# Kernel optimization log

Hardware: AMD Instinct MI355X
Metric: run time of the kernel (lower is better)

The kernel has to match this reference:

```python
import jax, jax.numpy as jnp
import numpy as np

BATCH = 65536
INPUT_DIM = 128
NUM_KNOTS = 10
DEGREE = 3  # n_basis = NUM_KNOTS - DEGREE - 1 = 6


def bspline_basis(x, knots, degree):
    """Cox-de Boor B-spline basis, vectorized over all batch/feature entries.

    x: [B, D] (already clipped into [knots[0], knots[-1]))
    knots: [K] uniform knot vector
    returns: [B, D, K - degree - 1]
    """
    xe = x[..., None]                                            # [B, D, 1]
    # degree-0 indicator basis: [B, D, K-1]
    B = ((xe >= knots[:-1]) & (xe < knots[1:])).astype(x.dtype)
    for d in range(1, degree + 1):
        left_den = knots[d:-1] - knots[:-(d + 1)]                # [K-1-d]
        right_den = knots[d + 1:] - knots[1:-d]                  # [K-1-d]
        safe_l = jnp.where(left_den > 0, left_den, 1.0)
        safe_r = jnp.where(right_den > 0, right_den, 1.0)
        left = jnp.where(left_den > 0, (xe - knots[:-(d + 1)]) / safe_l, 0.0) * B[..., :-1]
        right = jnp.where(right_den > 0, (knots[d + 1:] - xe) / safe_r, 0.0) * B[..., 1:]
        B = left + right                                          # [B, D, K-1-d]
    return B


def setup_inputs() -> dict:
    key = jax.random.key(0)
    k1, k2 = jax.random.split(key)
    x = jax.random.normal(k1, (BATCH, INPUT_DIM), dtype=jnp.float32)
    interaction_weights = jax.random.normal(k2, (INPUT_DIM, INPUT_DIM), dtype=jnp.float32)
    return {"x": x, "interaction_weights": interaction_weights}


def reference(x, interaction_weights):
    # Shared uniform knot vector over [-1, 1], identical across all features
    knots = jnp.linspace(-1.0, 1.0, NUM_KNOTS).astype(x.dtype)
    eps = 1e-6
    xc = jnp.clip(x, knots[0], knots[-1] - eps)
    basis = bspline_basis(xc, knots, DEGREE)                     # [B, D, 6]
    B_sz = x.shape[0]
    basis_flat = basis.reshape(B_sz, -1)                         # [B, D*6]
    # interaction: out[b, j] = sum_i x[b,i]^2 * sigmoid(W[i,j])
    # (equivalent to bmm(x^T, x * sigmoid(W)) in the original, without
    #  materializing the [B, D, D] broadcast intermediate)
    S = jax.nn.sigmoid(interaction_weights)                      # [D, D]
    interaction = (x * x) @ S                                    # [B, D]
    return jnp.concatenate([basis_flat, interaction], axis=1)    # [B, D*6 + D]
```

## Files before the change

kernel.cpp:

```cpp
#include <hip/hip_runtime.h>
#include <math.h>

#define BATCH 65536
#define DIM 128
#define NBAS 6
#define OUTW 896
#define ROWS_PER_TILE 32
#define CHROWS 8
#define NCHUNK 4
#define XT_F 128
#define BAS_F 768

typedef float f4v __attribute__((ext_vector_type(4)));

__global__ __launch_bounds__(256) void sigmoid_k(const float* __restrict__ W,
                                                 float* __restrict__ S) {
    int t = blockIdx.x * 256 + threadIdx.x;
    float w = W[t];
    S[t] = 1.0f / (1.0f + expf(-w));
}

__device__ __forceinline__ void bw(float x, int& s,
                                   float& w0, float& w1, float& w2, float& w3) {
    const float i6 = 0.16666666666666666f;
    float xc = fminf(fmaxf(x, -1.0f), 1.0f - 1e-6f);
    float p  = (xc + 1.0f) * 4.5f;
    float sf = floorf(p);
    float u  = p - sf;
    s = (int)sf;
    float u2 = u * u;
    float v  = 1.0f - u;
    w0 = u * u2 * i6;
    w1 = (((-3.0f * u + 3.0f) * u + 3.0f) * u + 1.0f) * i6;
    w2 = ((3.0f * u - 6.0f) * u2 + 4.0f) * i6;
    w3 = v * v * v * i6;
}

__global__ __launch_bounds__(256, 4) void kan_main(const float* __restrict__ X,
                                                   const float* __restrict__ S,
                                                   float* __restrict__ out) {
    __shared__ __align__(16) float xTf[ROWS_PER_TILE * XT_F];
    __shared__ __align__(16) float bas[CHROWS * BAS_F];

    const int tid = threadIdx.x;
    const int row0 = blockIdx.x * ROWS_PER_TILE;

    const float4* X4 = (const float4*)(X + (size_t)row0 * DIM);
    float4* xT4 = (float4*)xTf;
#pragma unroll
    for (int k = 0; k < 4; ++k) {
        int e4 = k * 256 + tid;
        xT4[e4] = X4[e4];
    }
    f4v z4 = {0.0f, 0.0f, 0.0f, 0.0f};
    f4v* bas4 = (f4v*)bas;
#pragma unroll
    for (int k = 0; k < 6; ++k) bas4[k * 256 + tid] = z4;
    __syncthreads();

    {
        const int c = tid & 31;
        const int r0 = (tid >> 5) * 4;

        float acc[4][4];
#pragma unroll
        for (int rr = 0; rr < 4; ++rr)
#pragma unroll
            for (int q = 0; q < 4; ++q) acc[rr][q] = 0.0f;

        const float4* S4 = (const float4*)S;
        const float* xp0 = xTf + (r0 + 0) * XT_F;
        const float* xp1 = xTf + (r0 + 1) * XT_F;
        const float* xp2 = xTf + (r0 + 2) * XT_F;
        const float* xp3 = xTf + (r0 + 3) * XT_F;
#pragma unroll 2
        for (int i = 0; i < DIM; ++i) {
            float4 s = S4[i * 32 + c];
            float x0 = xp0[i], x1 = xp1[i], x2 = xp2[i], x3 = xp3[i];
            float xq[4] = {x0 * x0, x1 * x1, x2 * x2, x3 * x3};
#pragma unroll
            for (int rr = 0; rr < 4; ++rr) {
#pragma unroll
                for (int q = 0; q < 4; ++q) {
                    float sv = (q == 0) ? s.x : (q == 1) ? s.y : (q == 2) ? s.z : s.w;
                    acc[rr][q] = fmaf(xq[rr], sv, acc[rr][q]);
                }
            }
        }

#pragma unroll
        for (int rr = 0; rr < 4; ++rr) {
            f4v v = {acc[rr][0], acc[rr][1], acc[rr][2], acc[rr][3]};
            __builtin_nontemporal_store(
                v, (f4v*)(out + (size_t)(row0 + r0 + rr) * OUTW + DIM * NBAS + 4 * c));
        }
    }

    {
        const int sr = tid >> 5;
        const int f0 = tid & 31;
        for (int c = 0; c < NCHUNK; ++c) {
            const float* xrow = xTf + (c * CHROWS + sr) * XT_F;
            float* basr = bas + sr * BAS_F;
#pragma unroll
            for (int m = 0; m < 4; ++m) {
                int f = f0 + 32 * m;
                float x = xrow[f];
                int s;
                float w0, w1, w2, w3;
                bw(x, s, w0, w1, w2, w3);
                float* bp = basr + f * NBAS + s;
                if (s <= 5)           bp[0]  = w0;
                if (s >= 1 && s <= 6) bp[-1] = w1;
                if (s >= 2 && s <= 7) bp[-2] = w2;
                if (s >= 3)           bp[-3] = w3;
            }
            __syncthreads();

            float* ob = out + (size_t)(row0 + c * CHROWS) * OUTW;
#pragma unroll
            for (int k = 0; k < 6; ++k) {
                int idx = k * 256 + tid;
                int r = idx / 192;
                int j = idx - r * 192;
                f4v v = bas4[idx];
                __builtin_nontemporal_store(v, (f4v*)(ob + (size_t)r * OUTW + 4 * j));
                bas4[idx] = z4;
            }
            __syncthreads();
        }
    }
}

extern "C" void kernel_launch(void* const* d_in, const int* in_sizes, int n_in,
                              void* d_out, int out_size, void* d_ws, size_t ws_size,
                              hipStream_t stream) {
    const float* X = (const float*)d_in[0];
    const float* W = (const float*)d_in[1];
    float* out = (float*)d_out;
    float* S = (float*)d_ws;

    sigmoid_k<<<(DIM * DIM) / 256, 256, 0, stream>>>(W, S);
    kan_main<<<BATCH / ROWS_PER_TILE, 256, 0, stream>>>(X, S, out);
}
```

Before: 284.5 us.

## Compute interaction matmul with fp16 MFMA instead of scalar FMAs

Replaces the scalar fp32 FMA loop for (x*x)@sigmoid(W) with MFMA 16x16x32 f16 instructions. The sigmoid kernel now writes a transposed fp16 copy of S, and squared inputs are staged as fp16 in a swizzled shared buffer. This cuts the ALU work of the interaction part but lowers precision to fp16 inputs, adds shared memory, and reduces launch-bound occupancy from 4 to 3. Output stores become scalar per element rather than float4.

```diff
diff --git a/kernel.cpp b/kernel.cpp
--- a/kernel.cpp
+++ b/kernel.cpp
@@ -12,12 +12,18 @@
 #define BAS_F 768
 
 typedef float f4v __attribute__((ext_vector_type(4)));
+typedef float f32x4 __attribute__((ext_vector_type(4)));
+typedef _Float16 f16x4 __attribute__((ext_vector_type(4)));
+typedef _Float16 f16x8 __attribute__((ext_vector_type(8)));
 
-__global__ __launch_bounds__(256) void sigmoid_k(const float* __restrict__ W,
-                                                 float* __restrict__ S) {
+__global__ __launch_bounds__(256) void sigmoid_kT(const float* __restrict__ W,
+                                                  _Float16* __restrict__ ST) {
     int t = blockIdx.x * 256 + threadIdx.x;
+    int i = t >> 7;
+    int j = t & 127;
     float w = W[t];
-    S[t] = 1.0f / (1.0f + expf(-w));
+    float s = 1.0f / (1.0f + expf(-w));
+    ST[j * 128 + i] = (_Float16)s;
 }
 
 __device__ __forceinline__ void bw(float x, int& s,
@@ -36,10 +42,11 @@
     w3 = v * v * v * i6;
 }
 
-__global__ __launch_bounds__(256, 4) void kan_main(const float* __restrict__ X,
-                                                   const float* __restrict__ S,
+__global__ __launch_bounds__(256, 3) void kan_main(const float* __restrict__ X,
+                                                   const _Float16* __restrict__ ST,
                                                    float* __restrict__ out) {
     __shared__ __align__(16) float xTf[ROWS_PER_TILE * XT_F];
+    __shared__ __align__(16) _Float16 xsq[ROWS_PER_TILE * 128];
     __shared__ __align__(16) float bas[CHROWS * BAS_F];
 
     const int tid = threadIdx.x;
@@ -50,7 +57,14 @@
 #pragma unroll
     for (int k = 0; k < 4; ++k) {
         int e4 = k * 256 + tid;
-        xT4[e4] = X4[e4];
+        int r = e4 >> 5;
+        int i4 = e4 & 31;
+        float4 xv = X4[e4];
+        xT4[e4] = xv;
+        f16x4 q = {(_Float16)(xv.x * xv.x), (_Float16)(xv.y * xv.y),
+                   (_Float16)(xv.z * xv.z), (_Float16)(xv.w * xv.w)};
+        int byte = (r * 256 + i4 * 8) ^ ((r & 7) << 4);
+        *(f16x4*)((char*)xsq + byte) = q;
     }
     f4v z4 = {0.0f, 0.0f, 0.0f, 0.0f};
     f4v* bas4 = (f4v*)bas;
@@ -59,40 +73,43 @@
     __syncthreads();
 
     {
-        const int c = tid & 31;
-        const int r0 = (tid >> 5) * 4;
+        const int w = tid >> 6, l = tid & 63;
+        const int lr = l & 15, lg = l >> 4;
+        const int rt = w & 1;
+        const int ch = w >> 1;
 
-        float acc[4][4];
+        f16x8 af[4];
 #pragma unroll
-        for (int rr = 0; rr < 4; ++rr)
+        for (int kk = 0; kk < 4; ++kk) {
+            int byte = ((rt * 16 + lr) * 256 + kk * 64 + lg * 16) ^ ((lr & 7) << 4);
+            af[kk] = *(const f16x8*)((const char*)xsq + byte);
+        }
+
+        f32x4 acc[4];
 #pragma unroll
-            for (int q = 0; q < 4; ++q) acc[rr][q] = 0.0f;
+        for (int ct = 0; ct < 4; ++ct) acc[ct] = (f32x4){0.f, 0.f, 0.f, 0.f};
 
-        const float4* S4 = (const float4*)S;
-        const float* xp0 = xTf + (r0 + 0) * XT_F;
-        const float* xp1 = xTf + (r0 + 1) * XT_F;
-        const float* xp2 = xTf + (r0 + 2) * XT_F;
-        const float* xp3 = xTf + (r0 + 3) * XT_F;
-#pragma unroll 2
-        for (int i = 0; i < DIM; ++i) {
-            float4 s = S4[i * 32 + c];
-            float x0 = xp0[i], x1 = xp1[i], x2 = xp2[i], x3 = xp3[i];
-            float xq[4] = {x0 * x0, x1 * x1, x2 * x2, x3 * x3};
+        const char* stb = (const char*)ST;
 #pragma unroll
-            for (int rr = 0; rr < 4; ++rr) {
+        for (int ct = 0; ct < 4; ++ct) {
+            const char* bp = stb + (ch * 64 + ct * 16 + lr) * 256 + lg * 16;
 #pragma unroll
-                for (int q = 0; q < 4; ++q) {
-                    float sv = (q == 0) ? s.x : (q == 1) ? s.y : (q == 2) ? s.z : s.w;
-                    acc[rr][q] = fmaf(xq[rr], sv, acc[rr][q]);
-                }
+            for (int kk = 0; kk < 4; ++kk) {
+                f16x8 bf = *(const f16x8*)(bp + kk * 64);
+                acc[ct] = __builtin_amdgcn_mfma_f32_16x16x32_f16(af[kk], bf, acc[ct], 0, 0, 0);
             }
         }
 
 #pragma unroll
-        for (int rr = 0; rr < 4; ++rr) {
-            f4v v = {acc[rr][0], acc[rr][1], acc[rr][2], acc[rr][3]};
-            __builtin_nontemporal_store(
-                v, (f4v*)(out + (size_t)(row0 + r0 + rr) * OUTW + DIM * NBAS + 4 * c));
+        for (int ct = 0; ct < 4; ++ct) {
+            int colb = ch * 64 + ct * 16 + lr;
+#pragma unroll
+            for (int q = 0; q < 4; ++q) {
+                int rowi = rt * 16 + lg * 4 + q;
+                __builtin_nontemporal_store(
+                    acc[ct][q],
+                    out + (size_t)(row0 + rowi) * OUTW + DIM * NBAS + colb);
+            }
         }
     }
 
@@ -138,8 +155,8 @@
     const float* X = (const float*)d_in[0];
     const float* W = (const float*)d_in[1];
     float* out = (float*)d_out;
-    float* S = (float*)d_ws;
+    _Float16* ST = (_Float16*)d_ws;
 
-    sigmoid_k<<<(DIM * DIM) / 256, 256, 0, stream>>>(W, S);
-    kan_main<<<BATCH / ROWS_PER_TILE, 256, 0, stream>>>(X, S, out);
+    sigmoid_kT<<<(DIM * DIM) / 256, 256, 0, stream>>>(W, ST);
+    kan_main<<<BATCH / ROWS_PER_TILE, 256, 0, stream>>>(X, ST, out);
 }
```

After: 269.8 us. -5.2%, faster.
